# Kernel optimization log

Measured on AMD Instinct MI355X. Metric: run time of the kernel, lower is better.

The kernel has to match this reference:

```python
import jax, jax.numpy as jnp
import numpy as np

E = 512   # embed_size
H = 8     # num_heads
D = E // H
N = 4
T = 2048


def quantize(x, b, e):
    # fake-quant: scale by 2^e, clamp to signed b-bit range, floor, dequant
    s = jnp.exp2(e)
    lo = -jnp.exp2(b - 1.0)
    hi = jnp.exp2(b - 1.0) - 1.0
    return jnp.floor(jnp.clip(x / s, lo, hi)) * s


def setup_inputs() -> dict:
    key = jax.random.key(0)
    ks = jax.random.split(key, 8)
    f = lambda k, shape: jax.random.normal(k, shape, dtype=jnp.float32)
    w = 1.0 / np.sqrt(E)  # ~ torch Linear init scale
    return {
        "values": f(ks[0], (N, T, E)),
        "keys": f(ks[1], (N, T, E)),
        "query": f(ks[2], (N, T, E)),
        "Wq": f(ks[3], (E, E)) * w, "bq": jnp.zeros((E,), jnp.float32),
        "Wk": f(ks[4], (E, E)) * w, "bk": jnp.zeros((E,), jnp.float32),
        "Wv": f(ks[5], (E, E)) * w, "bv": jnp.zeros((E,), jnp.float32),
        "Wo": f(ks[6], (E, E)) * w, "bo": jnp.zeros((E,), jnp.float32),
        "b_param": jnp.float32(8.0),
        "e_param": jnp.float32(0.0),
    }


def reference(values, keys, query, Wq, bq, Wk, bk, Wv, bv, Wo, bo, b_param, e_param):
    n, t, emb = query.shape
    d = emb // H
    # linear projections (torch Linear: x @ W^T + b), split heads -> [N,H,T,D]
    q = (query @ Wq.T + bq).reshape(n, t, H, d).transpose(0, 2, 1, 3)
    k = (keys @ Wk.T + bk).reshape(n, t, H, d).transpose(0, 2, 1, 3)
    v = (values @ Wv.T + bv).reshape(n, t, H, d).transpose(0, 2, 1, 3)
    b = jnp.clip(b_param, 1.0, 8.0)
    q = quantize(q, b, e_param)
    k = quantize(k, b, e_param)
    v = quantize(v, b, e_param)
    # NOTE: source scales by sqrt(embed_size), not sqrt(head_dim)
    energy = jnp.einsum('nhqd,nhkd->nhqk', q, k) / jnp.sqrt(jnp.float32(emb))
    attn = jax.nn.softmax(energy, axis=-1)
    out = jnp.einsum('nhqk,nhkd->nhqd', attn, v)
    out = out.transpose(0, 2, 1, 3).reshape(n, t, emb)
    return out @ Wo.T + bo
```

## Files before the change

### kernel.cpp

```cpp
#include <hip/hip_runtime.h>
#include <hip/hip_bf16.h>
#include <hip/hip_fp16.h>
#include <cstdint>
#include <cstddef>


typedef __attribute__((ext_vector_type(8))) _Float16 f16x8;
typedef __attribute__((ext_vector_type(2))) __fp16 hf16x2;
typedef __attribute__((ext_vector_type(16))) float f32x16;
typedef __attribute__((ext_vector_type(4))) unsigned u32x4;
typedef unsigned short u16;

#define EL  4194304
#define WEL 262144

static __device__ __forceinline__ u16 f2h(float x) {
  _Float16 h = (_Float16)x;
  return __builtin_bit_cast(u16, h);
}
static __device__ __forceinline__ unsigned pkh2(float a, float b) {
  hf16x2 p = __builtin_amdgcn_cvt_pkrtz(a, b);
  return __builtin_bit_cast(unsigned, p);
}
static __device__ __forceinline__ void gl_lds16(const void* g, void* l) {
  __builtin_amdgcn_global_load_lds(
      (__attribute__((address_space(1))) void*)g,
      (__attribute__((address_space(3))) void*)l, 16, 0, 0);
}

struct PrepAllArgs { const float* src[7]; };

__global__ __launch_bounds__(256) void prep_all_kernel(PrepAllArgs a,
                                                       u16* __restrict__ dst)
{
  const int i = blockIdx.x * 256 + threadIdx.x;
  const float* src; int off;
  if (i < 3145728) {
    const int m = i >> 20; off = i & 1048575;
    src = (m == 0) ? a.src[0] : (m == 1) ? a.src[1] : a.src[2];
  } else {
    const int j = i - 3145728; const int w = j >> 16; off = j & 65535;
    src = (w == 0) ? a.src[3] : (w == 1) ? a.src[4]
        : (w == 2) ? a.src[5] : a.src[6];
  }
  const float4 v = ((const float4*)src)[off];
  ushort4 o;
  o.x = f2h(v.x); o.y = f2h(v.y); o.z = f2h(v.z); o.w = f2h(v.w);
  ((ushort4*)dst)[i] = o;
}

struct ProjArgs {
  const u16* X[3]; const u16* W[3]; const float* bias[3];
  u16* dst[3]; int trans[3];
};

__global__ __launch_bounds__(256, 3) void proj_kernel(ProjArgs args,
    const float* __restrict__ bparam, const float* __restrict__ eparam)
{
  __shared__ u16 sm[17408];
  u16* const As = sm;
  u16* const Bs = sm + 8192;

  const int z = blockIdx.z;
  const u16* __restrict__ X = args.X[z];
  const u16* __restrict__ W = args.W[z];
  const float* __restrict__ bias = args.bias[z];
  u16* __restrict__ dst = args.dst[z];
  const int mode = args.trans[z];

  const int tid  = threadIdx.x;
  const int lane = tid & 63;
  const int wave = tid >> 6;
  const int lam  = lane & 31;
  const int hl   = lane >> 5;
  const int wm   = wave & 1;
  const int wn   = wave >> 1;
  const int mbase = blockIdx.x * 128;
  const int nbase = blockIdx.y * 128;

  const int srow = tid >> 3;
  const int sj   = (tid & 7) ^ (srow & 7);
  const u16* gA = X + (size_t)(mbase + srow) * 512 + sj * 8;
  const u16* gB = W + (size_t)(nbase + srow) * 512 + sj * 8;

  int offA[2][4], offB[2][4];
#pragma unroll
  for (int f = 0; f < 2; ++f)
#pragma unroll
    for (int kk = 0; kk < 4; ++kk) {
      const int c = 2 * kk + hl;
      const int m = wm * 64 + f * 32 + lam;
      offA[f][kk] = m * 128 + ((c ^ (m & 7)) * 16);
      const int nn = wn * 64 + f * 32 + lam;
      offB[f][kk] = nn * 128 + ((c ^ (nn & 7)) * 16);
    }

  f32x16 acc[2][2];
#pragma unroll
  for (int a = 0; a < 2; ++a)
#pragma unroll
    for (int b = 0; b < 2; ++b)
#pragma unroll
      for (int i = 0; i < 16; ++i) acc[a][b][i] = 0.f;

  for (int kt = 0; kt < 512; kt += 64) {
    __syncthreads();
#pragma unroll
    for (int t = 0; t < 4; ++t) {
      gl_lds16(gA + kt + t * 32 * 512, (char*)As + tid * 16 + t * 4096);
      gl_lds16(gB + kt + t * 32 * 512, (char*)Bs + tid * 16 + t * 4096);
    }
    __syncthreads();

    f16x8 fA[2][4], fB[2][4];
#pragma unroll
    for (int f = 0; f < 2; ++f)
#pragma unroll
      for (int kk = 0; kk < 4; ++kk) {
        fA[f][kk] = *(const f16x8*)((const char*)As + offA[f][kk]);
        fB[f][kk] = *(const f16x8*)((const char*)Bs + offB[f][kk]);
      }
#pragma unroll
    for (int mf = 0; mf < 2; ++mf)
#pragma unroll
      for (int nf = 0; nf < 2; ++nf)
#pragma unroll
        for (int kk = 0; kk < 4; ++kk)
          acc[mf][nf] = __builtin_amdgcn_mfma_f32_32x32x16_f16(
              fA[mf][kk], fB[nf][kk], acc[mf][nf], 0, 0, 0);
  }

  const float bq   = fminf(fmaxf(bparam[0], 1.0f), 8.0f);
  const float e    = eparam[0];
  const float s    = exp2f(e);
  const float invs = exp2f(-e);
  const float qlo  = -exp2f(bq - 1.0f);
  const float qhi  = exp2f(bq - 1.0f) - 1.0f;
  const int nidx = mbase >> 11;
  const int tb   = mbase & 2047;
  const int hb   = nbase >> 6;

  if (mode == 0) {
    const float SCQ = (float)(1.4426950408889634 / 22.627416997969522);
#pragma unroll
    for (int mf = 0; mf < 2; ++mf)
#pragma unroll
      for (int nf = 0; nf < 2; ++nf)
#pragma unroll
        for (int reg = 0; reg < 16; ++reg) {
          int col = wn * 64 + nf * 32 + lam;
          int row = wm * 64 + mf * 32 + (reg & 3) + 8 * (reg >> 2) + 4 * hl;
          float v = acc[mf][nf][reg] + bias[nbase + col];
          float qv = floorf(fminf(fmaxf(v * invs, qlo), qhi)) * s;
          dst[((size_t)(nidx * 8 + hb + (col >> 6)) * 2048 + tb + row) * 64 +
              (col & 63)] = f2h(qv * SCQ);
        }
  } else if (mode == 1) {
#pragma unroll
    for (int mf = 0; mf < 2; ++mf)
#pragma unroll
      for (int nf = 0; nf < 2; ++nf)
#pragma unroll
        for (int reg = 0; reg < 16; ++reg) {
          int col = wn * 64 + nf * 32 + lam;
          int row = wm * 64 + mf * 32 + (reg & 3) + 8 * (reg >> 2) + 4 * hl;
          float v = acc[mf][nf][reg] + bias[nbase + col];
          float qv = floorf(fminf(fmaxf(v * invs, qlo), qhi)) * s;
          const int t = tb + row;
          const int d = col & 63;
          dst[(size_t)(nidx * 8 + hb + (col >> 6)) * 131072 +
              (t >> 5) * 2048 + (t & 31) * 64 + (((d >> 3) ^ (t & 7)) << 3) +
              (d & 7)] = f2h(qv);
        }
  } else {
    __syncthreads();
#pragma unroll
    for (int mf = 0; mf < 2; ++mf)
#pragma unroll
      for (int nf = 0; nf < 2; ++nf)
#pragma unroll
        for (int reg = 0; reg < 16; ++reg) {
          int col = wn * 64 + nf * 32 + lam;
          int row = wm * 64 + mf * 32 + (reg & 3) + 8 * (reg >> 2) + 4 * hl;
          float v = acc[mf][nf][reg] + bias[nbase + col];
          float qv = floorf(fminf(fmaxf(v * invs, qlo), qhi)) * s;
          sm[col * 136 + row] = f2h(qv);
        }
    __syncthreads();
    const int r = tid >> 1, half = tid & 1;
    const u16* sp = sm + r * 136 + half * 64;
    const int d  = r & 63;
    const int sb = d & 1;
    const int rx = (d >> 1) & 7;
    u16* const gp0 = dst + (size_t)(nidx * 8 + hb + (r >> 6)) * 131072 +
                     (d >> 1) * 64;
#pragma unroll
    for (int kb = 0; kb < 2; ++kb) {
      const int Bg = ((tb + half * 64) >> 5) + kb;
#pragma unroll
      for (int g = 0; g < 4; ++g) {
        const int qoff = (g & 1) * 4 + (g >> 1) * 16;
        const uint2 lo = *(const uint2*)(sp + kb * 32 + qoff);
        const uint2 hi = *(const uint2*)(sp + kb * 32 + qoff + 8);
        uint4 val; val.x = lo.x; val.y = lo.y; val.z = hi.x; val.w = hi.y;
        const int s2 = ((g << 1) | sb) ^ rx;
        *(uint4*)(gp0 + Bg * 2048 + s2 * 8) = val;
      }
    }
  }
}

__global__ __launch_bounds__(256, 2) void attn_kernel(
    const u16* __restrict__ qbuf, const u16* __restrict__ kbuf,
    const u16* __restrict__ vtbuf, u16* __restrict__ ctx)
{
  __shared__ u16 sm[17920];
  char* const smc = (char*)sm;

  const int tid  = threadIdx.x;
  const int wave = tid >> 6;
  const int lane = tid & 63;
  const int lam  = lane & 31;
  const int hl   = lane >> 5;
  const int bid = blockIdx.x;
  const int wg  = (bid & 7) * 128 + (bid >> 3);
  const int qt = wg & 31;
  const int nh = wg >> 5;
  const int hd = nh & 7;
  const int n  = nh >> 3;
  const int qbase = qt * 64;

  const u16* Qp = qbuf + ((size_t)nh * 2048 + qbase) * 64;
  const u16* gK = kbuf  + (size_t)nh * 131072 + wave * 2048 + lane * 8;
  const u16* gV = vtbuf + (size_t)nh * 131072 + wave * 2048 + lane * 8;
  char* const kvb = smc + wave * 8192;

  f16x8 qf[2][4];
#pragma unroll
  for (int qb = 0; qb < 2; ++qb)
#pragma unroll
    for (int dk = 0; dk < 4; ++dk)
      qf[qb][dk] = *(const f16x8*)(Qp + (qb * 32 + lam) * 64 + dk * 16 + hl * 8);
#pragma unroll
  for (int qb = 0; qb < 2; ++qb)
#pragma unroll
    for (int dk = 0; dk < 4; ++dk)
      asm volatile("" :: "v"(qf[qb][dk]));

  auto stage4 = [&](const u16* src, char* dstb) {
#pragma unroll
    for (int r = 0; r < 4; ++r)
      gl_lds16(src + r * 512, dstb + r * 1024 + lane * 16);
  };

  stage4(gK, kvb);
  stage4(gV, kvb + 4096);

  int offK[4];
#pragma unroll
  for (int dk = 0; dk < 4; ++dk)
    offK[dk] = lam * 128 + (((2 * dk + hl) ^ (lam & 7)) << 4);
  int offV[2][2];
#pragma unroll
  for (int nf = 0; nf < 2; ++nf)
#pragma unroll
    for (int kkl = 0; kkl < 2; ++kkl) {
      const int R = nf * 16 + (lam >> 1);
      const int s2 = (((2 * kkl + hl) << 1) | (lam & 1)) ^ (R & 7);
      offV[nf][kkl] = 4096 + R * 128 + s2 * 16;
    }

  float l_acc[2] = {0.f, 0.f};
  f32x16 O[2][2];
#pragma unroll
  for (int a = 0; a < 2; ++a)
#pragma unroll
    for (int b = 0; b < 2; ++b)
#pragma unroll
      for (int i = 0; i < 16; ++i) O[a][b][i] = 0.f;

  for (int t = 0; t < 16; ++t) {
    asm volatile("s_waitcnt vmcnt(4)" ::: "memory");
    f16x8 Kf[4];
#pragma unroll
    for (int dk = 0; dk < 4; ++dk)
      Kf[dk] = *(const f16x8*)(kvb + offK[dk]);
    asm volatile("s_waitcnt lgkmcnt(0)" ::: "memory");
    stage4(gK + ((t + 1) & 15) * 8192, kvb);

    f16x8 pfrag[2][2];
#pragma unroll
    for (int qb = 0; qb < 2; ++qb) {
      f32x16 S;
#pragma unroll
      for (int i = 0; i < 16; ++i) S[i] = 0.f;
      __builtin_amdgcn_s_setprio(1);
#pragma unroll
      for (int dk = 0; dk < 4; ++dk)
        S = __builtin_amdgcn_mfma_f32_32x32x16_f16(Kf[dk], qf[qb][dk],
                                                   S, 0, 0, 0);
      __builtin_amdgcn_s_setprio(0);
      u32x4 fr[2];
#pragma unroll
      for (int gh = 0; gh < 4; ++gh) {
        float p0 = __builtin_amdgcn_exp2f(S[4 * gh + 0]);
        float p1 = __builtin_amdgcn_exp2f(S[4 * gh + 1]);
        float p2 = __builtin_amdgcn_exp2f(S[4 * gh + 2]);
        float p3 = __builtin_amdgcn_exp2f(S[4 * gh + 3]);
        l_acc[qb] += (p0 + p1) + (p2 + p3);
        fr[gh >> 1][(gh & 1) * 2 + 0] = pkh2(p0, p1);
        fr[gh >> 1][(gh & 1) * 2 + 1] = pkh2(p2, p3);
      }
      pfrag[qb][0] = __builtin_bit_cast(f16x8, fr[0]);
      pfrag[qb][1] = __builtin_bit_cast(f16x8, fr[1]);
    }

    asm volatile("s_waitcnt vmcnt(4)" ::: "memory");
    f16x8 Vf[2][2];
#pragma unroll
    for (int nf = 0; nf < 2; ++nf)
#pragma unroll
      for (int kkl = 0; kkl < 2; ++kkl)
        Vf[nf][kkl] = *(const f16x8*)(kvb + offV[nf][kkl]);
    asm volatile("s_waitcnt lgkmcnt(0)" ::: "memory");
    stage4(gV + ((t + 1) & 15) * 8192, kvb + 4096);

    __builtin_amdgcn_s_setprio(1);
#pragma unroll
    for (int qb = 0; qb < 2; ++qb)
#pragma unroll
      for (int nf = 0; nf < 2; ++nf)
#pragma unroll
        for (int kkl = 0; kkl < 2; ++kkl)
          O[qb][nf] = __builtin_amdgcn_mfma_f32_32x32x16_f16(
              pfrag[qb][kkl], Vf[nf][kkl], O[qb][nf], 0, 0, 0);
    __builtin_amdgcn_s_setprio(0);
  }

  asm volatile("s_waitcnt vmcnt(0)" ::: "memory");
#pragma unroll
  for (int qb = 0; qb < 2; ++qb) l_acc[qb] += __shfl_xor(l_acc[qb], 32);
  float* lred = (float*)(smc + 34816);
  if (hl == 0) {
    lred[wave * 64 + lam]      = l_acc[0];
    lred[wave * 64 + 32 + lam] = l_acc[1];
  }
  __syncthreads();

  const int q  = tid >> 3;
  const int dc = (tid & 7) * 8;
#pragma unroll
  for (int qb = 0; qb < 2; ++qb) {
    float* Ow = (float*)(smc + wave * 8704);
#pragma unroll
    for (int nf = 0; nf < 2; ++nf)
#pragma unroll
      for (int r = 0; r < 16; ++r) {
        const int qrow = (r & 3) + 8 * (r >> 2) + 4 * hl;
        Ow[qrow * 68 + nf * 32 + lam] = O[qb][nf][r];
      }
    __syncthreads();
    float a[8];
    {
      const char* b = smc + q * 272 + dc * 4;
      const float4 v0 = *(const float4*)b;
      const float4 v1 = *(const float4*)(b + 16);
      a[0] = v0.x; a[1] = v0.y; a[2] = v0.z; a[3] = v0.w;
      a[4] = v1.x; a[5] = v1.y; a[6] = v1.z; a[7] = v1.w;
    }
#pragma unroll
    for (int w = 1; w < 4; ++w) {
      const char* b = smc + w * 8704 + q * 272 + dc * 4;
      const float4 v0 = *(const float4*)b;
      const float4 v1 = *(const float4*)(b + 16);
      a[0] += v0.x; a[1] += v0.y; a[2] += v0.z; a[3] += v0.w;
      a[4] += v1.x; a[5] += v1.y; a[6] += v1.z; a[7] += v1.w;
    }
    const float lsum = lred[qb * 32 + q] + lred[64 + qb * 32 + q] +
                       lred[128 + qb * 32 + q] + lred[192 + qb * 32 + q];
    const float rinv = 1.0f / lsum;
    unsigned outp[4];
#pragma unroll
    for (int i = 0; i < 4; ++i)
      outp[i] = pkh2(a[2 * i] * rinv, a[2 * i + 1] * rinv);
    u16* cp = ctx + ((size_t)n * 2048 + qbase + qb * 32 + q) * 512 +
              hd * 64 + dc;
    *(uint4*)cp = *(const uint4*)outp;
    if (qb == 0) __syncthreads();
  }
}

__global__ __launch_bounds__(256) void outproj_kernel(
    const u16* __restrict__ ctxb, const u16* __restrict__ Wof,
    const float* __restrict__ bias, float* __restrict__ out)
{
  __shared__ u16 sm[12288];
  u16* const As = sm;
  u16* const Bs = sm + 4096;

  const int tid  = threadIdx.x;
  const int lane = tid & 63;
  const int wave = tid >> 6;
  const int lam  = lane & 31;
  const int hl   = lane >> 5;
  const int wm   = wave & 1;
  const int wn   = wave >> 1;
  const int mbase = blockIdx.x * 64;
  const int nbase = blockIdx.y * 128;

  const int srow = tid >> 3;
  const int sj   = (tid & 7) ^ (srow & 7);
  const u16* gA = ctxb + (size_t)(mbase + srow) * 512 + sj * 8;
  const u16* gB = Wof  + (size_t)(nbase + srow) * 512 + sj * 8;

  int offA[4], offB[2][4];
#pragma unroll
  for (int kk = 0; kk < 4; ++kk) {
    const int c = 2 * kk + hl;
    const int m = wm * 32 + lam;
    offA[kk] = m * 128 + ((c ^ (m & 7)) * 16);
#pragma unroll
    for (int f = 0; f < 2; ++f) {
      const int nn = wn * 64 + f * 32 + lam;
      offB[f][kk] = nn * 128 + ((c ^ (nn & 7)) * 16);
    }
  }

  f32x16 acc[2];
#pragma unroll
  for (int a = 0; a < 2; ++a)
#pragma unroll
    for (int i = 0; i < 16; ++i) acc[a][i] = 0.f;

  for (int kt = 0; kt < 512; kt += 64) {
    __syncthreads();
#pragma unroll
    for (int t = 0; t < 2; ++t)
      gl_lds16(gA + kt + t * 32 * 512, (char*)As + tid * 16 + t * 4096);
#pragma unroll
    for (int t = 0; t < 4; ++t)
      gl_lds16(gB + kt + t * 32 * 512, (char*)Bs + tid * 16 + t * 4096);
    __syncthreads();

    f16x8 fA[4], fB[2][4];
#pragma unroll
    for (int kk = 0; kk < 4; ++kk) {
      fA[kk] = *(const f16x8*)((const char*)As + offA[kk]);
#pragma unroll
      for (int f = 0; f < 2; ++f)
        fB[f][kk] = *(const f16x8*)((const char*)Bs + offB[f][kk]);
    }
#pragma unroll
    for (int nf = 0; nf < 2; ++nf)
#pragma unroll
      for (int kk = 0; kk < 4; ++kk)
        acc[nf] = __builtin_amdgcn_mfma_f32_32x32x16_f16(
            fA[kk], fB[nf][kk], acc[nf], 0, 0, 0);
  }

#pragma unroll
  for (int nf = 0; nf < 2; ++nf)
#pragma unroll
    for (int reg = 0; reg < 16; ++reg) {
      int col = nbase + wn * 64 + nf * 32 + lam;
      int row = mbase + wm * 32 + (reg & 3) + 8 * (reg >> 2) + 4 * hl;
      out[(size_t)row * 512 + col] = acc[nf][reg] + bias[col];
    }
}

extern "C" void kernel_launch(void* const* d_in, const int* in_sizes, int n_in,
                              void* d_out, int out_size, void* d_ws, size_t ws_size,
                              hipStream_t stream) {
  (void)in_sizes; (void)n_in; (void)out_size; (void)ws_size;
  const float* values = (const float*)d_in[0];
  const float* keys   = (const float*)d_in[1];
  const float* query  = (const float*)d_in[2];
  const float* Wq = (const float*)d_in[3];  const float* bq = (const float*)d_in[4];
  const float* Wk = (const float*)d_in[5];  const float* bk = (const float*)d_in[6];
  const float* Wv = (const float*)d_in[7];  const float* bv = (const float*)d_in[8];
  const float* Wo = (const float*)d_in[9];  const float* bo = (const float*)d_in[10];
  const float* bp = (const float*)d_in[11]; const float* ep = (const float*)d_in[12];

  u16* ws    = (u16*)d_ws;
  u16* qbuf  = ws;
  u16* kbuf  = ws + (size_t)EL;
  u16* vtbuf = ws + (size_t)2 * EL;
  u16* ctx   = ws + (size_t)3 * EL;
  u16* xwf   = ws + (size_t)4 * EL;

  PrepAllArgs pa;
  pa.src[0] = query; pa.src[1] = keys; pa.src[2] = values;
  pa.src[3] = Wq; pa.src[4] = Wk; pa.src[5] = Wv; pa.src[6] = Wo;
  prep_all_kernel<<<13312, 256, 0, stream>>>(pa, xwf);

  const float* Bsrc[3] = {bq, bk, bv};
  u16* Dst[3] = {qbuf, kbuf, vtbuf};
  ProjArgs a;
  for (int m = 0; m < 3; ++m) {
    a.X[m] = xwf + (size_t)m * EL;
    a.W[m] = xwf + (size_t)3 * EL + (size_t)m * WEL;
    a.bias[m] = Bsrc[m]; a.dst[m] = Dst[m]; a.trans[m] = m;
  }
  proj_kernel<<<dim3(64, 4, 3), 256, 0, stream>>>(a, bp, ep);

  attn_kernel<<<dim3(1024), 256, 0, stream>>>(qbuf, kbuf, vtbuf, ctx);
  outproj_kernel<<<dim3(128, 4), 256, 0, stream>>>(
      ctx, xwf + (size_t)3 * EL + (size_t)3 * WEL, bo, (float*)d_out);
}
```

Measured before the change: 186.3 us.

## Split attention waves across query halves and KV halves with shared double-buffered tiles

Each wave now handles 32 query rows and half of each 64-key tile, instead of all 64 query rows over a private quarter of the keys. K/V tiles are staged block-wide into a double-buffered LDS region, with a barrier per iteration. This halves per-wave accumulators and Q fragments, so launch bounds are raised to four blocks per SM for more occupancy. The cost is a block barrier every tile and twice as many loop iterations, in exchange for lower register pressure and a simpler final cross-wave reduction.

Result: faster. 181.1 us (-2.8%).

```diff
diff --git a/kernel.cpp b/kernel.cpp
--- a/kernel.cpp
+++ b/kernel.cpp
@@ -210,11 +210,11 @@
   }
 }
 
-__global__ __launch_bounds__(256, 2) void attn_kernel(
+__global__ __launch_bounds__(256, 4) void attn_kernel(
     const u16* __restrict__ qbuf, const u16* __restrict__ kbuf,
     const u16* __restrict__ vtbuf, u16* __restrict__ ctx)
 {
-  __shared__ u16 sm[17920];
+  __shared__ u16 sm[17664];
   char* const smc = (char*)sm;
 
   const int tid  = threadIdx.x;
@@ -222,6 +222,8 @@
   const int lane = tid & 63;
   const int lam  = lane & 31;
   const int hl   = lane >> 5;
+  const int qh   = wave >> 1;
+  const int kw   = wave & 1;
   const int bid = blockIdx.x;
   const int wg  = (bid & 7) * 128 + (bid >> 3);
   const int qt = wg & 31;
@@ -230,36 +232,30 @@
   const int n  = nh >> 3;
   const int qbase = qt * 64;
 
-  const u16* Qp = qbuf + ((size_t)nh * 2048 + qbase) * 64;
-  const u16* gK = kbuf  + (size_t)nh * 131072 + wave * 2048 + lane * 8;
-  const u16* gV = vtbuf + (size_t)nh * 131072 + wave * 2048 + lane * 8;
-  char* const kvb = smc + wave * 8192;
-
-  f16x8 qf[2][4];
-#pragma unroll
-  for (int qb = 0; qb < 2; ++qb)
-#pragma unroll
-    for (int dk = 0; dk < 4; ++dk)
-      qf[qb][dk] = *(const f16x8*)(Qp + (qb * 32 + lam) * 64 + dk * 16 + hl * 8);
-#pragma unroll
-  for (int qb = 0; qb < 2; ++qb)
-#pragma unroll
-    for (int dk = 0; dk < 4; ++dk)
-      asm volatile("" :: "v"(qf[qb][dk]));
-
-  auto stage4 = [&](const u16* src, char* dstb) {
-#pragma unroll
-    for (int r = 0; r < 4; ++r)
-      gl_lds16(src + r * 512, dstb + r * 1024 + lane * 16);
+  const u16* Qp = qbuf + ((size_t)nh * 2048 + qbase + qh * 32) * 64;
+  const u16* gK = kbuf  + (size_t)nh * 131072;
+  const u16* gV = vtbuf + (size_t)nh * 131072;
+
+  f16x8 qf[4];
+#pragma unroll
+  for (int dk = 0; dk < 4; ++dk)
+    qf[dk] = *(const f16x8*)(Qp + lam * 64 + dk * 16 + hl * 8);
+#pragma unroll
+  for (int dk = 0; dk < 4; ++dk)
+    asm volatile("" :: "v"(qf[dk]));
+
+  auto stage = [&](int tn, char* db) {
+    const int e = tn * 4096 + tid * 8;
+    gl_lds16(gK + e,        db + tid * 16);
+    gl_lds16(gK + e + 2048, db + 4096 + tid * 16);
+    gl_lds16(gV + e,        db + 8192 + tid * 16);
+    gl_lds16(gV + e + 2048, db + 12288 + tid * 16);
   };
 
-  stage4(gK, kvb);
-  stage4(gV, kvb + 4096);
-
   int offK[4];
 #pragma unroll
   for (int dk = 0; dk < 4; ++dk)
-    offK[dk] = lam * 128 + (((2 * dk + hl) ^ (lam & 7)) << 4);
+    offK[dk] = kw * 4096 + lam * 128 + (((2 * dk + hl) ^ (lam & 7)) << 4);
   int offV[2][2];
 #pragma unroll
   for (int nf = 0; nf < 2; ++nf)
@@ -267,127 +263,111 @@
     for (int kkl = 0; kkl < 2; ++kkl) {
       const int R = nf * 16 + (lam >> 1);
       const int s2 = (((2 * kkl + hl) << 1) | (lam & 1)) ^ (R & 7);
-      offV[nf][kkl] = 4096 + R * 128 + s2 * 16;
-    }
-
-  float l_acc[2] = {0.f, 0.f};
-  f32x16 O[2][2];
-#pragma unroll
-  for (int a = 0; a < 2; ++a)
-#pragma unroll
-    for (int b = 0; b < 2; ++b)
-#pragma unroll
-      for (int i = 0; i < 16; ++i) O[a][b][i] = 0.f;
-
-  for (int t = 0; t < 16; ++t) {
-    asm volatile("s_waitcnt vmcnt(4)" ::: "memory");
+      offV[nf][kkl] = 8192 + kw * 4096 + R * 128 + s2 * 16;
+    }
+
+  float l_acc = 0.f;
+  f32x16 O[2];
+#pragma unroll
+  for (int b = 0; b < 2; ++b)
+#pragma unroll
+    for (int i = 0; i < 16; ++i) O[b][i] = 0.f;
+
+  stage(0, smc);
+
+  for (int t = 0; t < 32; ++t) {
+    asm volatile("s_waitcnt vmcnt(0)" ::: "memory");
+    __builtin_amdgcn_s_barrier();
+    __builtin_amdgcn_sched_barrier(0);
+    stage((t + 1) & 31, smc + (((t + 1) & 1) << 14));
+
+    const char* bb = smc + ((t & 1) << 14);
     f16x8 Kf[4];
 #pragma unroll
     for (int dk = 0; dk < 4; ++dk)
-      Kf[dk] = *(const f16x8*)(kvb + offK[dk]);
-    asm volatile("s_waitcnt lgkmcnt(0)" ::: "memory");
-    stage4(gK + ((t + 1) & 15) * 8192, kvb);
-
-    f16x8 pfrag[2][2];
-#pragma unroll
-    for (int qb = 0; qb < 2; ++qb) {
-      f32x16 S;
-#pragma unroll
-      for (int i = 0; i < 16; ++i) S[i] = 0.f;
-      __builtin_amdgcn_s_setprio(1);
-#pragma unroll
-      for (int dk = 0; dk < 4; ++dk)
-        S = __builtin_amdgcn_mfma_f32_32x32x16_f16(Kf[dk], qf[qb][dk],
-                                                   S, 0, 0, 0);
-      __builtin_amdgcn_s_setprio(0);
-      u32x4 fr[2];
-#pragma unroll
-      for (int gh = 0; gh < 4; ++gh) {
-        float p0 = __builtin_amdgcn_exp2f(S[4 * gh + 0]);
-        float p1 = __builtin_amdgcn_exp2f(S[4 * gh + 1]);
-        float p2 = __builtin_amdgcn_exp2f(S[4 * gh + 2]);
-        float p3 = __builtin_amdgcn_exp2f(S[4 * gh + 3]);
-        l_acc[qb] += (p0 + p1) + (p2 + p3);
-        fr[gh >> 1][(gh & 1) * 2 + 0] = pkh2(p0, p1);
-        fr[gh >> 1][(gh & 1) * 2 + 1] = pkh2(p2, p3);
-      }
-      pfrag[qb][0] = __builtin_bit_cast(f16x8, fr[0]);
-      pfrag[qb][1] = __builtin_bit_cast(f16x8, fr[1]);
-    }
-
-    asm volatile("s_waitcnt vmcnt(4)" ::: "memory");
+      Kf[dk] = *(const f16x8*)(bb + offK[dk]);
+
+    f32x16 S;
+#pragma unroll
+    for (int i = 0; i < 16; ++i) S[i] = 0.f;
+    __builtin_amdgcn_s_setprio(1);
+#pragma unroll
+    for (int dk = 0; dk < 4; ++dk)
+      S = __builtin_amdgcn_mfma_f32_32x32x16_f16(Kf[dk], qf[dk], S, 0, 0, 0);
+    __builtin_amdgcn_s_setprio(0);
+
+    u32x4 fr[2];
+#pragma unroll
+    for (int gh = 0; gh < 4; ++gh) {
+      float p0 = __builtin_amdgcn_exp2f(S[4 * gh + 0]);
+      float p1 = __builtin_amdgcn_exp2f(S[4 * gh + 1]);
+      float p2 = __builtin_amdgcn_exp2f(S[4 * gh + 2]);
+      float p3 = __builtin_amdgcn_exp2f(S[4 * gh + 3]);
+      l_acc += (p0 + p1) + (p2 + p3);
+      fr[gh >> 1][(gh & 1) * 2 + 0] = pkh2(p0, p1);
+      fr[gh >> 1][(gh & 1) * 2 + 1] = pkh2(p2, p3);
+    }
+    f16x8 pf0 = __builtin_bit_cast(f16x8, fr[0]);
+    f16x8 pf1 = __builtin_bit_cast(f16x8, fr[1]);
+
     f16x8 Vf[2][2];
 #pragma unroll
     for (int nf = 0; nf < 2; ++nf)
 #pragma unroll
       for (int kkl = 0; kkl < 2; ++kkl)
-        Vf[nf][kkl] = *(const f16x8*)(kvb + offV[nf][kkl]);
-    asm volatile("s_waitcnt lgkmcnt(0)" ::: "memory");
-    stage4(gV + ((t + 1) & 15) * 8192, kvb + 4096);
+        Vf[nf][kkl] = *(const f16x8*)(bb + offV[nf][kkl]);
 
     __builtin_amdgcn_s_setprio(1);
 #pragma unroll
-    for (int qb = 0; qb < 2; ++qb)
-#pragma unroll
-      for (int nf = 0; nf < 2; ++nf)
-#pragma unroll
-        for (int kkl = 0; kkl < 2; ++kkl)
-          O[qb][nf] = __builtin_amdgcn_mfma_f32_32x32x16_f16(
-              pfrag[qb][kkl], Vf[nf][kkl], O[qb][nf], 0, 0, 0);
+    for (int nf = 0; nf < 2; ++nf) {
+      O[nf] = __builtin_amdgcn_mfma_f32_32x32x16_f16(pf0, Vf[nf][0],
+                                                     O[nf], 0, 0, 0);
+      O[nf] = __builtin_amdgcn_mfma_f32_32x32x16_f16(pf1, Vf[nf][1],
+                                                     O[nf], 0, 0, 0);
+    }
     __builtin_amdgcn_s_setprio(0);
   }
 
   asm volatile("s_waitcnt vmcnt(0)" ::: "memory");
-#pragma unroll
-  for (int qb = 0; qb < 2; ++qb) l_acc[qb] += __shfl_xor(l_acc[qb], 32);
+  l_acc += __shfl_xor(l_acc, 32);
   float* lred = (float*)(smc + 34816);
-  if (hl == 0) {
-    lred[wave * 64 + lam]      = l_acc[0];
-    lred[wave * 64 + 32 + lam] = l_acc[1];
-  }
+  if (hl == 0) lred[wave * 32 + lam] = l_acc;
   __syncthreads();
 
-  const int q  = tid >> 3;
-  const int dc = (tid & 7) * 8;
-#pragma unroll
-  for (int qb = 0; qb < 2; ++qb) {
-    float* Ow = (float*)(smc + wave * 8704);
-#pragma unroll
-    for (int nf = 0; nf < 2; ++nf)
-#pragma unroll
-      for (int r = 0; r < 16; ++r) {
-        const int qrow = (r & 3) + 8 * (r >> 2) + 4 * hl;
-        Ow[qrow * 68 + nf * 32 + lam] = O[qb][nf][r];
-      }
-    __syncthreads();
-    float a[8];
-    {
-      const char* b = smc + q * 272 + dc * 4;
-      const float4 v0 = *(const float4*)b;
-      const float4 v1 = *(const float4*)(b + 16);
-      a[0] = v0.x; a[1] = v0.y; a[2] = v0.z; a[3] = v0.w;
-      a[4] = v1.x; a[5] = v1.y; a[6] = v1.z; a[7] = v1.w;
-    }
-#pragma unroll
-    for (int w = 1; w < 4; ++w) {
-      const char* b = smc + w * 8704 + q * 272 + dc * 4;
-      const float4 v0 = *(const float4*)b;
-      const float4 v1 = *(const float4*)(b + 16);
-      a[0] += v0.x; a[1] += v0.y; a[2] += v0.z; a[3] += v0.w;
-      a[4] += v1.x; a[5] += v1.y; a[6] += v1.z; a[7] += v1.w;
-    }
-    const float lsum = lred[qb * 32 + q] + lred[64 + qb * 32 + q] +
-                       lred[128 + qb * 32 + q] + lred[192 + qb * 32 + q];
-    const float rinv = 1.0f / lsum;
-    unsigned outp[4];
-#pragma unroll
-    for (int i = 0; i < 4; ++i)
-      outp[i] = pkh2(a[2 * i] * rinv, a[2 * i + 1] * rinv);
-    u16* cp = ctx + ((size_t)n * 2048 + qbase + qb * 32 + q) * 512 +
-              hd * 64 + dc;
-    *(uint4*)cp = *(const uint4*)outp;
-    if (qb == 0) __syncthreads();
-  }
+  float* Ow = (float*)(smc + wave * 8704);
+#pragma unroll
+  for (int nf = 0; nf < 2; ++nf)
+#pragma unroll
+    for (int r = 0; r < 16; ++r) {
+      const int qrow = (r & 3) + 8 * (r >> 2) + 4 * hl;
+      Ow[qrow * 68 + nf * 32 + lam] = O[nf][r];
+    }
+  __syncthreads();
+
+  const int q  = tid >> 2;
+  const int dc = (tid & 3) * 16;
+  const int qh2 = q >> 5;
+  float a[16];
+  {
+    const char* b0 = smc + (qh2 * 2) * 8704 + (q & 31) * 272 + dc * 4;
+    const char* b1 = b0 + 8704;
+#pragma unroll
+    for (int j = 0; j < 4; ++j) {
+      const float4 v0 = *(const float4*)(b0 + j * 16);
+      const float4 v1 = *(const float4*)(b1 + j * 16);
+      a[4 * j + 0] = v0.x + v1.x; a[4 * j + 1] = v0.y + v1.y;
+      a[4 * j + 2] = v0.z + v1.z; a[4 * j + 3] = v0.w + v1.w;
+    }
+  }
+  const float lsum = lred[qh2 * 64 + (q & 31)] + lred[qh2 * 64 + 32 + (q & 31)];
+  const float rinv = 1.0f / lsum;
+  unsigned outp[8];
+#pragma unroll
+  for (int i = 0; i < 8; ++i)
+    outp[i] = pkh2(a[2 * i] * rinv, a[2 * i + 1] * rinv);
+  u16* cp = ctx + ((size_t)n * 2048 + qbase + q) * 512 + hd * 64 + dc;
+  *(uint4*)cp       = *(const uint4*)&outp[0];
+  *(uint4*)(cp + 8) = *(const uint4*)&outp[4];
 }
 
 __global__ __launch_bounds__(256) void outproj_kernel(
```
